# Optimization experiments

Hardware: AMD Instinct MI355X
Metric: run time of the kernel (lower is better)

## Reference

```python
import jax, jax.numpy as jnp
import numpy as np

N_NODES = 100000


def gcn_conv(x, edge_index, W, b):
    """PyG-style GCNConv: x' = D^-1/2 (A+I) D^-1/2 (x W) + b (self-loops added)."""
    n = x.shape[0]
    h = x @ W  # [N, out]
    loop = jnp.arange(n, dtype=edge_index.dtype)
    src = jnp.concatenate([edge_index[0], loop])  # [E+N]
    dst = jnp.concatenate([edge_index[1], loop])
    deg = jax.ops.segment_sum(jnp.ones_like(dst, dtype=h.dtype), dst, num_segments=n)
    dinv = jnp.where(deg > 0, jax.lax.rsqrt(deg), 0.0)
    norm = dinv[src] * dinv[dst]  # [E+N]
    # gather -> scale -> scatter-add aggregation
    out = jax.ops.segment_sum(norm[:, None] * h[src], dst, num_segments=n)
    return out + b


def setup_inputs() -> dict:
    key = jax.random.key(0)
    k1, k2, k3, k4 = jax.random.split(key, 4)
    n, e = N_NODES, 2560000
    x = jax.random.normal(k1, (n, 2), dtype=jnp.float32)
    edge_index = jax.random.randint(k2, (2, e), 0, n, dtype=jnp.int32)
    hidden = 32
    W1 = jax.random.normal(k3, (2, hidden), dtype=jnp.float32) * (1.0 / np.sqrt(2))
    b1 = jnp.zeros((hidden,), dtype=jnp.float32)
    W2 = jax.random.normal(k4, (hidden, 1), dtype=jnp.float32) * (1.0 / np.sqrt(hidden))
    b2 = jnp.zeros((1,), dtype=jnp.float32)
    return {"x": x, "edge_index": edge_index, "W1": W1, "b1": b1, "W2": W2, "b2": b2}


def reference(x, edge_index, W1, b1, W2, b2):
    h = jax.nn.relu(gcn_conv(x, edge_index, W1, b1))
    return gcn_conv(h, edge_index, W2, b2)  # [N, 1]
```

## Files before the change

kernel.cpp:

```cpp
#include <hip/hip_runtime.h>


#define NBMAX 1024
#define NRMAX 32
#define AGG_BLKS 16
#define CHUNK 4096
#define NCHP 640
#define DBITS 12
#define DMASK 4095
#define NOEDGE 0xFFFFFFFFu


__device__ __forceinline__ int block_scan_excl(int v, int tid, int* wtot ) {
    int lane = tid & 63, w = tid >> 6;
    int inc = v;
#pragma unroll
    for (int d = 1; d < 64; d <<= 1) {
        int u = __shfl_up(inc, d);
        if (lane >= d) inc += u;
    }
    if (lane == 63) wtot[w] = inc;
    __syncthreads();
    if (w == 0) {
        int t = (lane < 16) ? wtot[lane] : 0;
#pragma unroll
        for (int d = 1; d < 16; d <<= 1) {
            int u = __shfl_up(t, d);
            if (lane >= d) t += u;
        }
        if (lane < 16) wtot[lane] = t;
        if (lane == 15) wtot[16] = t;
    }
    __syncthreads();
    int base = (w > 0) ? wtot[w - 1] : 0;
    return base + inc - v;
}


__global__ void k_px(const float2* __restrict__ x, const int* __restrict__ pdeg,
                     float* __restrict__ dinv, float2* __restrict__ px, int n) {
    int i = blockIdx.x * blockDim.x + threadIdx.x;
    if (i >= n) return;
    int deg = 1;
#pragma unroll
    for (int b = 0; b < AGG_BLKS; ++b) deg += pdeg[b * n + i];
    float d = rsqrtf((float)deg);
    dinv[i] = d;
    float2 xv = x[i];
    px[i] = make_float2(d * xv.x, d * xv.y);
}

__global__ void k_node(const float2* __restrict__ px, const float2* __restrict__ pP,
                       const float* __restrict__ dinv,
                       const float* __restrict__ W1, const float* __restrict__ b1,
                       const float* __restrict__ W2, float* __restrict__ s, int n) {
    int i = blockIdx.x * blockDim.x + threadIdx.x;
    if (i >= n) return;
    float2 v = px[i];
    float ax = v.x, ay = v.y;
#pragma unroll
    for (int b = 0; b < AGG_BLKS; ++b) {
        float2 p = pP[b * n + i];
        ax += p.x; ay += p.y;
    }
    float d = dinv[i];
    float dot = 0.f;
#pragma unroll
    for (int j = 0; j < 32; ++j) {
        float acc = fmaf(ax, W1[j], ay * W1[32 + j]);
        float h = fmaxf(fmaf(d, acc, b1[j]), 0.f);
        dot = fmaf(h, W2[j], dot);
    }
    s[i] = d * dot;
}

__global__ void k_out(const float* __restrict__ s, const float* __restrict__ ps,
                      const float* __restrict__ dinv, const float* __restrict__ b2,
                      float* __restrict__ out, int n) {
    int i = blockIdx.x * blockDim.x + threadIdx.x;
    if (i >= n) return;
    float acc = s[i];
#pragma unroll
    for (int b = 0; b < AGG_BLKS; ++b) acc += ps[b * n + i];
    out[i] = dinv[i] * acc + b2[0];
}


__global__ void k_cnt(const int* __restrict__ src, const int* __restrict__ dst,
                      int* __restrict__ cntT, int e, int NS, int NB) {
    __shared__ int h[NBMAX];
    for (int t = threadIdx.x; t < NB; t += blockDim.x) h[t] = 0;
    __syncthreads();
    int c0 = blockIdx.x * CHUNK, c1 = min(c0 + CHUNK, e);
    int len = c1 - c0, lq = len >> 2;
    const int4* d4 = (const int4*)(dst + c0);
    const int4* s4 = (const int4*)(src + c0);
    for (int j = threadIdx.x; j < lq; j += blockDim.x) {
        int4 dv = d4[j], sv = s4[j];
        atomicAdd(&h[(dv.x >> DBITS) * NS + (sv.x >> DBITS)], 1);
        atomicAdd(&h[(dv.y >> DBITS) * NS + (sv.y >> DBITS)], 1);
        atomicAdd(&h[(dv.z >> DBITS) * NS + (sv.z >> DBITS)], 1);
        atomicAdd(&h[(dv.w >> DBITS) * NS + (sv.w >> DBITS)], 1);
    }
    if (threadIdx.x == 0)
        for (int i = lq * 4; i < len; ++i)
            atomicAdd(&h[(dst[c0 + i] >> DBITS) * NS + (src[c0 + i] >> DBITS)], 1);
    __syncthreads();
    for (int t = threadIdx.x; t < NB; t += blockDim.x)
        cntT[blockIdx.x * NBMAX + t] = h[t];
}

__global__ __launch_bounds__(1024)
void k_scanA(int* __restrict__ cntT, int* __restrict__ tot, int NCH) {
    __shared__ int wtot[17];
    int bin = blockIdx.x, tid = threadIdx.x;
    int v = (tid < NCH) ? cntT[tid * NBMAX + bin] : 0;
    int ex = block_scan_excl(v, tid, wtot);
    if (tid < NCH) cntT[tid * NBMAX + bin] = ex;
    if (tid == 0) tot[bin] = wtot[16];
}

__global__ __launch_bounds__(1024)
void k_scanB(const int* __restrict__ tot, int* __restrict__ gbin,
             int* __restrict__ rbase, int* __restrict__ rlenp,
             unsigned* __restrict__ packed, int NB, int NS) {
    __shared__ int wtot[17];
    int tid = threadIdx.x;
    int t = (tid < NB) ? tot[tid] : 0;
    int p = (t + 3) & ~3;
    int gb = block_scan_excl(p, tid, wtot);
    int totalp = wtot[16];
    if (tid < NB) {
        gbin[tid] = gb;
        for (int k = t; k < p; ++k) packed[gb + k] = NOEDGE;
    }
    __syncthreads();
    if (tid < NB && (tid % NS) == 0) {
        int r = tid / NS;
        rbase[r] = gb;
        int nxt = (tid + NS < NB) ? gbin[tid + NS] : totalp;
        rlenp[r] = nxt - gb;
    }
}

__global__ __launch_bounds__(1024)
void k_bscatter(const int* __restrict__ src, const int* __restrict__ dst,
                const int* __restrict__ ofsT, const int* __restrict__ tot,
                const int* __restrict__ gbin, unsigned* __restrict__ packed,
                int e, int NS, int NB, int NCH) {
    __shared__ int curx[NBMAX], gba[NBMAX];
    __shared__ unsigned sbuf[CHUNK];
    __shared__ int dest[CHUNK];
    __shared__ int wtot[17];
    int blk = blockIdx.x, tid = threadIdx.x;
    int c0 = blk * CHUNK, c1 = min(c0 + CHUNK, e);
    int len = c1 - c0, lq = len >> 2;
    int cur = 0, hv = 0;
    if (tid < NB) {
        cur = ofsT[blk * NBMAX + tid];
        int nxt = (blk + 1 < NCH) ? ofsT[(blk + 1) * NBMAX + tid] : tot[tid];
        hv = nxt - cur;
    }
    int lo = block_scan_excl(hv, tid, wtot);
    if (tid < NB) {
        curx[tid] = lo;
        gba[tid] = gbin[tid] + cur - lo;
    }
    __syncthreads();
    const int4* d4 = (const int4*)(dst + c0);
    const int4* s4 = (const int4*)(src + c0);
    for (int j = tid; j < lq; j += blockDim.x) {
        int4 dv = d4[j], sv = s4[j];
        {
            int b = (dv.x >> DBITS) * NS + (sv.x >> DBITS);
            int sl = atomicAdd(&curx[b], 1);
            sbuf[sl] = ((unsigned)sv.x << DBITS) | (unsigned)(dv.x & DMASK);
            dest[sl] = gba[b] + sl;
        }
        {
            int b = (dv.y >> DBITS) * NS + (sv.y >> DBITS);
            int sl = atomicAdd(&curx[b], 1);
            sbuf[sl] = ((unsigned)sv.y << DBITS) | (unsigned)(dv.y & DMASK);
            dest[sl] = gba[b] + sl;
        }
        {
            int b = (dv.z >> DBITS) * NS + (sv.z >> DBITS);
            int sl = atomicAdd(&curx[b], 1);
            sbuf[sl] = ((unsigned)sv.z << DBITS) | (unsigned)(dv.z & DMASK);
            dest[sl] = gba[b] + sl;
        }
        {
            int b = (dv.w >> DBITS) * NS + (sv.w >> DBITS);
            int sl = atomicAdd(&curx[b], 1);
            sbuf[sl] = ((unsigned)sv.w << DBITS) | (unsigned)(dv.w & DMASK);
            dest[sl] = gba[b] + sl;
        }
    }
    if (tid == 0)
        for (int i = lq * 4; i < len; ++i) {
            int d = dst[c0 + i], sx = src[c0 + i];
            int b = (d >> DBITS) * NS + (sx >> DBITS);
            int sl = atomicAdd(&curx[b], 1);
            sbuf[sl] = ((unsigned)sx << DBITS) | (unsigned)(d & DMASK);
            dest[sl] = gba[b] + sl;
        }
    __syncthreads();
    for (int t = tid; t < len; t += blockDim.x)
        packed[dest[t]] = sbuf[t];
}


__global__ __launch_bounds__(1024, 8)
void k_deg(const unsigned* __restrict__ packed, const int* __restrict__ rbase,
           const int* __restrict__ rlenp, int* __restrict__ pdeg, int n) {
    __shared__ int acc[DMASK + 1];
    int r = blockIdx.y, b = blockIdx.x;
    int rs_r = min(DMASK + 1, n - (r << DBITS));
    for (int t = threadIdx.x; t < rs_r; t += blockDim.x) acc[t] = 0;
    __syncthreads();
    int base = rbase[r], q = rlenp[r] >> 2;
    int qper = (q + gridDim.x - 1) / gridDim.x;
    int qlo = b * qper, qhi = min(qlo + qper, q);
    const uint4* p4 = (const uint4*)(packed + base);
    for (int j = qlo + threadIdx.x; j < qhi; j += blockDim.x) {
        uint4 v = p4[j];
        if (v.x != NOEDGE) atomicAdd(&acc[v.x & DMASK], 1);
        if (v.y != NOEDGE) atomicAdd(&acc[v.y & DMASK], 1);
        if (v.z != NOEDGE) atomicAdd(&acc[v.z & DMASK], 1);
        if (v.w != NOEDGE) atomicAdd(&acc[v.w & DMASK], 1);
    }
    __syncthreads();
    int nb = b * n + (r << DBITS);
    for (int t = threadIdx.x; t < rs_r; t += blockDim.x) pdeg[nb + t] = acc[t];
}

__global__ __launch_bounds__(1024, 8)
void k_agg1(const unsigned* __restrict__ packed, const int* __restrict__ rbase,
            const int* __restrict__ rlenp, const float2* __restrict__ px,
            float2* __restrict__ pP, int n) {
    __shared__ float acc[2 * (DMASK + 1)];
    int r = blockIdx.y, b = blockIdx.x;
    int rs_r = min(DMASK + 1, n - (r << DBITS));
    for (int t = threadIdx.x; t < 2 * rs_r; t += blockDim.x) acc[t] = 0.f;
    __syncthreads();
    int base = rbase[r], q = rlenp[r] >> 2;
    int qper = (q + gridDim.x - 1) / gridDim.x;
    int qlo = b * qper, qhi = min(qlo + qper, q);
    const uint4* p4 = (const uint4*)(packed + base);
    int nm1 = n - 1;
    for (int j = qlo + threadIdx.x; j < qhi; j += blockDim.x) {
        uint4 v = p4[j];
        int i0 = min((int)(v.x >> DBITS), nm1);
        int i1 = min((int)(v.y >> DBITS), nm1);
        int i2 = min((int)(v.z >> DBITS), nm1);
        int i3 = min((int)(v.w >> DBITS), nm1);
        float2 g0 = px[i0], g1 = px[i1], g2 = px[i2], g3 = px[i3];
        if (v.x != NOEDGE) { int d0 = (v.x & DMASK) * 2; atomicAdd(&acc[d0], g0.x); atomicAdd(&acc[d0 + 1], g0.y); }
        if (v.y != NOEDGE) { int d1 = (v.y & DMASK) * 2; atomicAdd(&acc[d1], g1.x); atomicAdd(&acc[d1 + 1], g1.y); }
        if (v.z != NOEDGE) { int d2 = (v.z & DMASK) * 2; atomicAdd(&acc[d2], g2.x); atomicAdd(&acc[d2 + 1], g2.y); }
        if (v.w != NOEDGE) { int d3 = (v.w & DMASK) * 2; atomicAdd(&acc[d3], g3.x); atomicAdd(&acc[d3 + 1], g3.y); }
    }
    __syncthreads();
    int nb = b * n + (r << DBITS);
    for (int t = threadIdx.x; t < rs_r; t += blockDim.x)
        pP[nb + t] = make_float2(acc[2 * t], acc[2 * t + 1]);
}

__global__ __launch_bounds__(1024, 8)
void k_agg2(const unsigned* __restrict__ packed, const int* __restrict__ rbase,
            const int* __restrict__ rlenp, const float* __restrict__ s,
            float* __restrict__ ps, int n) {
    __shared__ float acc[DMASK + 1];
    int r = blockIdx.y, b = blockIdx.x;
    int rs_r = min(DMASK + 1, n - (r << DBITS));
    for (int t = threadIdx.x; t < rs_r; t += blockDim.x) acc[t] = 0.f;
    __syncthreads();
    int base = rbase[r], q = rlenp[r] >> 2;
    int qper = (q + gridDim.x - 1) / gridDim.x;
    int qlo = b * qper, qhi = min(qlo + qper, q);
    const uint4* p4 = (const uint4*)(packed + base);
    int nm1 = n - 1;
    for (int j = qlo + threadIdx.x; j < qhi; j += blockDim.x) {
        uint4 v = p4[j];
        int i0 = min((int)(v.x >> DBITS), nm1);
        int i1 = min((int)(v.y >> DBITS), nm1);
        int i2 = min((int)(v.z >> DBITS), nm1);
        int i3 = min((int)(v.w >> DBITS), nm1);
        float g0 = s[i0], g1 = s[i1], g2 = s[i2], g3 = s[i3];
        if (v.x != NOEDGE) atomicAdd(&acc[v.x & DMASK], g0);
        if (v.y != NOEDGE) atomicAdd(&acc[v.y & DMASK], g1);
        if (v.z != NOEDGE) atomicAdd(&acc[v.z & DMASK], g2);
        if (v.w != NOEDGE) atomicAdd(&acc[v.w & DMASK], g3);
    }
    __syncthreads();
    int nb = b * n + (r << DBITS);
    for (int t = threadIdx.x; t < rs_r; t += blockDim.x) ps[nb + t] = acc[t];
}


__global__ void f_zero(int* __restrict__ ideg, float2* __restrict__ P, int n) {
    int i = blockIdx.x * blockDim.x + threadIdx.x;
    if (i < n) { ideg[i] = 0; P[i] = make_float2(0.f, 0.f); }
}
__global__ void f_count(const int* __restrict__ dst, int* __restrict__ ideg, int e) {
    int i = blockIdx.x * blockDim.x + threadIdx.x;
    if (i < e) atomicAdd(&ideg[dst[i]], 1);
}
__global__ void f_px(const float2* __restrict__ x, const int* __restrict__ ideg,
                     float* __restrict__ dinv, float2* __restrict__ px, int n) {
    int i = blockIdx.x * blockDim.x + threadIdx.x;
    if (i >= n) return;
    float d = rsqrtf((float)(1 + ideg[i]));
    dinv[i] = d;
    float2 xv = x[i];
    px[i] = make_float2(d * xv.x, d * xv.y);
}
__global__ void f_scatter_px(const int* __restrict__ src, const int* __restrict__ dst,
                             const float2* __restrict__ px, float* __restrict__ Pf, int e) {
    int i = blockIdx.x * blockDim.x + threadIdx.x;
    if (i >= e) return;
    int sidx = src[i], d = dst[i];
    float2 v = px[sidx];
    atomicAdd(&Pf[2 * d], v.x);
    atomicAdd(&Pf[2 * d + 1], v.y);
}
__global__ void f_node(const float2* __restrict__ px, const float2* __restrict__ P,
                       const float* __restrict__ dinv,
                       const float* __restrict__ W1, const float* __restrict__ b1,
                       const float* __restrict__ W2,
                       float* __restrict__ s, float* __restrict__ S, int n) {
    int i = blockIdx.x * blockDim.x + threadIdx.x;
    if (i >= n) return;
    float d = dinv[i];
    float2 v = px[i], p = P[i];
    float ax = v.x + p.x, ay = v.y + p.y;
    float dot = 0.f;
#pragma unroll
    for (int j = 0; j < 32; ++j) {
        float acc = fmaf(ax, W1[j], ay * W1[32 + j]);
        float h = fmaxf(fmaf(d, acc, b1[j]), 0.f);
        dot = fmaf(h, W2[j], dot);
    }
    float sv = d * dot;
    s[i] = sv;
    S[i] = sv;
}
__global__ void f_scatter_s(const int* __restrict__ src, const int* __restrict__ dst,
                            const float* __restrict__ s, float* __restrict__ S, int e) {
    int i = blockIdx.x * blockDim.x + threadIdx.x;
    if (i < e) atomicAdd(&S[dst[i]], s[src[i]]);
}
__global__ void f_out(const float* __restrict__ S, const float* __restrict__ dinv,
                      const float* __restrict__ b2, float* __restrict__ out, int n) {
    int i = blockIdx.x * blockDim.x + threadIdx.x;
    if (i < n) out[i] = dinv[i] * S[i] + b2[0];
}


extern "C" void kernel_launch(void* const* d_in, const int* in_sizes, int n_in,
                              void* d_out, int out_size, void* d_ws, size_t ws_size,
                              hipStream_t stream) {
    const float* x  = (const float*)d_in[0];
    const int*   ei = (const int*)d_in[1];
    const float* W1 = (const float*)d_in[2];
    const float* b1 = (const float*)d_in[3];
    const float* W2 = (const float*)d_in[4];
    const float* b2 = (const float*)d_in[5];
    float* out = (float*)d_out;

    int n = in_sizes[0] / 2;
    int e = in_sizes[1] / 2;
    const int* src = ei;
    const int* dst = ei + e;
    int NR  = (n + DMASK) >> DBITS;
    int NS  = NR;
    int NB  = NR * NS;
    int NCH = (e + CHUNK - 1) / CHUNK;

    char* ws = (char*)d_ws;
    auto align = [](size_t v) { return (v + 255) & ~(size_t)255; };
    size_t off = 0;
    float*  dinv = (float*) (ws + off); off = align(off + (size_t)n * 4);
    float2* px   = (float2*)(ws + off); off = align(off + (size_t)n * 8);
    float*  s    = (float*) (ws + off); off = align(off + (size_t)n * 4);
    int*    pdeg = (int*)   (ws + off); off = align(off + (size_t)AGG_BLKS * n * 4);
    float2* pP   = (float2*)(ws + off); off = align(off + (size_t)AGG_BLKS * n * 8);
    float*  ps   = (float*) (ws + off); off = align(off + (size_t)AGG_BLKS * n * 4);
    int*    rbase = (int*)(ws + off); off = align(off + NRMAX * 4);
    int*    rlenp = (int*)(ws + off); off = align(off + NRMAX * 4);
    int*    gbin  = (int*)(ws + off); off = align(off + NBMAX * 4);
    int*    tot   = (int*)(ws + off); off = align(off + NBMAX * 4);
    int*    cntT  = (int*)(ws + off); off = align(off + (size_t)NCHP * NBMAX * 4);
    unsigned* packed = (unsigned*)(ws + off);
    size_t need = off + (size_t)(e + 4 * NBMAX) * 4;

    const int B = 256;
    int gn = (n + B - 1) / B, ge = (e + B - 1) / B;

    bool fast = (need <= ws_size) && (NB <= NBMAX) && (NCH <= NCHP) && (NR <= NRMAX);

    if (fast) {
        dim3 ag(AGG_BLKS, NR);
        k_cnt     <<<NCH, B, 0, stream>>>(src, dst, cntT, e, NS, NB);
        k_scanA   <<<NB, 1024, 0, stream>>>(cntT, tot, NCH);
        k_scanB   <<<1, 1024, 0, stream>>>(tot, gbin, rbase, rlenp, packed, NB, NS);
        k_bscatter<<<NCH, 1024, 0, stream>>>(src, dst, cntT, tot, gbin, packed, e, NS, NB, NCH);
        k_deg     <<<ag, 1024, 0, stream>>>(packed, rbase, rlenp, pdeg, n);
        k_px      <<<gn, B, 0, stream>>>((const float2*)x, pdeg, dinv, px, n);
        k_agg1    <<<ag, 1024, 0, stream>>>(packed, rbase, rlenp, px, pP, n);
        k_node    <<<gn, B, 0, stream>>>(px, pP, dinv, W1, b1, W2, s, n);
        k_agg2    <<<ag, 1024, 0, stream>>>(packed, rbase, rlenp, s, ps, n);
        k_out     <<<gn, B, 0, stream>>>(s, ps, dinv, b2, out, n);
    } else {
        int*   ideg = pdeg;
        float2* P   = pP;
        float* S    = ps;
        f_zero      <<<gn, B, 0, stream>>>(ideg, P, n);
        f_count     <<<ge, B, 0, stream>>>(dst, ideg, e);
        f_px        <<<gn, B, 0, stream>>>((const float2*)x, ideg, dinv, px, n);
        f_scatter_px<<<ge, B, 0, stream>>>(src, dst, px, (float*)P, e);
        f_node      <<<gn, B, 0, stream>>>(px, P, dinv, W1, b1, W2, s, S, n);
        f_scatter_s <<<ge, B, 0, stream>>>(src, dst, s, S, e);
        f_out       <<<gn, B, 0, stream>>>(S, dinv, b2, out, n);
    }
}
```

Baseline: 110.2 us.

## Stage source-node windows in LDS for aggregation gathers via finer source binning

Source bins are narrowed to 2048 nodes (NS=49, NB=1225 bins), so each destination row's edges are grouped by source window. The aggregation kernels stage the matching px or s window into shared memory and read features from LDS instead of random global gathers. The price is more bins in the count, scan and scatter stages, a two-bins-per-thread scan, extra block syncs per window, and lower launch-bound occupancy hints for the aggregation kernels.

```diff
diff --git a/kernel.cpp b/kernel.cpp
--- a/kernel.cpp
+++ b/kernel.cpp
@@ -1,13 +1,15 @@
 #include <hip/hip_runtime.h>
 
 
-#define NBMAX 1024
+#define CSTR 1280
 #define NRMAX 32
 #define AGG_BLKS 16
 #define CHUNK 4096
 #define NCHP 640
 #define DBITS 12
 #define DMASK 4095
+#define SBITS 11
+#define SMASK 2047
 #define NOEDGE 0xFFFFFFFFu
 
 
@@ -88,7 +90,7 @@
 
 __global__ void k_cnt(const int* __restrict__ src, const int* __restrict__ dst,
                       int* __restrict__ cntT, int e, int NS, int NB) {
-    __shared__ int h[NBMAX];
+    __shared__ int h[CSTR];
     for (int t = threadIdx.x; t < NB; t += blockDim.x) h[t] = 0;
     __syncthreads();
     int c0 = blockIdx.x * CHUNK, c1 = min(c0 + CHUNK, e);
@@ -97,49 +99,57 @@
     const int4* s4 = (const int4*)(src + c0);
     for (int j = threadIdx.x; j < lq; j += blockDim.x) {
         int4 dv = d4[j], sv = s4[j];
-        atomicAdd(&h[(dv.x >> DBITS) * NS + (sv.x >> DBITS)], 1);
-        atomicAdd(&h[(dv.y >> DBITS) * NS + (sv.y >> DBITS)], 1);
-        atomicAdd(&h[(dv.z >> DBITS) * NS + (sv.z >> DBITS)], 1);
-        atomicAdd(&h[(dv.w >> DBITS) * NS + (sv.w >> DBITS)], 1);
+        atomicAdd(&h[(dv.x >> DBITS) * NS + (sv.x >> SBITS)], 1);
+        atomicAdd(&h[(dv.y >> DBITS) * NS + (sv.y >> SBITS)], 1);
+        atomicAdd(&h[(dv.z >> DBITS) * NS + (sv.z >> SBITS)], 1);
+        atomicAdd(&h[(dv.w >> DBITS) * NS + (sv.w >> SBITS)], 1);
     }
     if (threadIdx.x == 0)
         for (int i = lq * 4; i < len; ++i)
-            atomicAdd(&h[(dst[c0 + i] >> DBITS) * NS + (src[c0 + i] >> DBITS)], 1);
+            atomicAdd(&h[(dst[c0 + i] >> DBITS) * NS + (src[c0 + i] >> SBITS)], 1);
     __syncthreads();
     for (int t = threadIdx.x; t < NB; t += blockDim.x)
-        cntT[blockIdx.x * NBMAX + t] = h[t];
+        cntT[blockIdx.x * CSTR + t] = h[t];
 }
 
 __global__ __launch_bounds__(1024)
 void k_scanA(int* __restrict__ cntT, int* __restrict__ tot, int NCH) {
     __shared__ int wtot[17];
     int bin = blockIdx.x, tid = threadIdx.x;
-    int v = (tid < NCH) ? cntT[tid * NBMAX + bin] : 0;
+    int v = (tid < NCH) ? cntT[tid * CSTR + bin] : 0;
     int ex = block_scan_excl(v, tid, wtot);
-    if (tid < NCH) cntT[tid * NBMAX + bin] = ex;
+    if (tid < NCH) cntT[tid * CSTR + bin] = ex;
     if (tid == 0) tot[bin] = wtot[16];
 }
 
 __global__ __launch_bounds__(1024)
 void k_scanB(const int* __restrict__ tot, int* __restrict__ gbin,
              int* __restrict__ rbase, int* __restrict__ rlenp,
-             unsigned* __restrict__ packed, int NB, int NS) {
+             unsigned* __restrict__ packed, int NB, int NS, int NR) {
     __shared__ int wtot[17];
+    __shared__ int gball[2048];
     int tid = threadIdx.x;
-    int t = (tid < NB) ? tot[tid] : 0;
-    int p = (t + 3) & ~3;
-    int gb = block_scan_excl(p, tid, wtot);
-    int totalp = wtot[16];
-    if (tid < NB) {
-        gbin[tid] = gb;
-        for (int k = t; k < p; ++k) packed[gb + k] = NOEDGE;
-    }
-    __syncthreads();
-    if (tid < NB && (tid % NS) == 0) {
-        int r = tid / NS;
-        rbase[r] = gb;
-        int nxt = (tid + NS < NB) ? gbin[tid + NS] : totalp;
-        rlenp[r] = nxt - gb;
+    int b0 = 2 * tid, b1 = b0 + 1;
+    int t0 = (b0 < NB) ? tot[b0] : 0;
+    int t1 = (b1 < NB) ? tot[b1] : 0;
+    int p0 = (t0 + 3) & ~3, p1 = (t1 + 3) & ~3;
+    int ps = block_scan_excl(p0 + p1, tid, wtot);
+    int total = wtot[16];
+    if (b0 < NB) {
+        gbin[b0] = ps; gball[b0] = ps;
+        for (int k = t0; k < p0; ++k) packed[ps + k] = NOEDGE;
+    }
+    if (b1 < NB) {
+        int base1 = ps + p0;
+        gbin[b1] = base1; gball[b1] = base1;
+        for (int k = t1; k < p1; ++k) packed[base1 + k] = NOEDGE;
+    }
+    __syncthreads();
+    if (tid < NR) {
+        int base = gball[tid * NS];
+        int nxt = (tid + 1 < NR) ? gball[(tid + 1) * NS] : total;
+        rbase[tid] = base;
+        rlenp[tid] = nxt - base;
     }
 }
 
@@ -148,60 +158,64 @@
                 const int* __restrict__ ofsT, const int* __restrict__ tot,
                 const int* __restrict__ gbin, unsigned* __restrict__ packed,
                 int e, int NS, int NB, int NCH) {
-    __shared__ int curx[NBMAX], gba[NBMAX];
+    __shared__ int curx[CSTR], gba[CSTR];
     __shared__ unsigned sbuf[CHUNK];
     __shared__ int dest[CHUNK];
     __shared__ int wtot[17];
     int blk = blockIdx.x, tid = threadIdx.x;
     int c0 = blk * CHUNK, c1 = min(c0 + CHUNK, e);
     int len = c1 - c0, lq = len >> 2;
-    int cur = 0, hv = 0;
-    if (tid < NB) {
-        cur = ofsT[blk * NBMAX + tid];
-        int nxt = (blk + 1 < NCH) ? ofsT[(blk + 1) * NBMAX + tid] : tot[tid];
-        hv = nxt - cur;
-    }
-    int lo = block_scan_excl(hv, tid, wtot);
-    if (tid < NB) {
-        curx[tid] = lo;
-        gba[tid] = gbin[tid] + cur - lo;
-    }
+    int b0 = 2 * tid, b1 = b0 + 1;
+    int cur0 = 0, cur1 = 0, h0 = 0, h1 = 0;
+    if (b0 < NB) {
+        cur0 = ofsT[blk * CSTR + b0];
+        int nxt = (blk + 1 < NCH) ? ofsT[(blk + 1) * CSTR + b0] : tot[b0];
+        h0 = nxt - cur0;
+    }
+    if (b1 < NB) {
+        cur1 = ofsT[blk * CSTR + b1];
+        int nxt = (blk + 1 < NCH) ? ofsT[(blk + 1) * CSTR + b1] : tot[b1];
+        h1 = nxt - cur1;
+    }
+    int lo = block_scan_excl(h0 + h1, tid, wtot);
+    if (b0 < NB) { curx[b0] = lo;      gba[b0] = gbin[b0] + cur0 - lo; }
+    if (b1 < NB) { curx[b1] = lo + h0; gba[b1] = gbin[b1] + cur1 - (lo + h0); }
     __syncthreads();
     const int4* d4 = (const int4*)(dst + c0);
     const int4* s4 = (const int4*)(src + c0);
     for (int j = tid; j < lq; j += blockDim.x) {
         int4 dv = d4[j], sv = s4[j];
         {
-            int b = (dv.x >> DBITS) * NS + (sv.x >> DBITS);
+            int b = (dv.x >> DBITS) * NS + (sv.x >> SBITS);
             int sl = atomicAdd(&curx[b], 1);
-            sbuf[sl] = ((unsigned)sv.x << DBITS) | (unsigned)(dv.x & DMASK);
+            sbuf[sl] = ((unsigned)(sv.x & SMASK) << DBITS) | (unsigned)(dv.x & DMASK);
             dest[sl] = gba[b] + sl;
         }
         {
-            int b = (dv.y >> DBITS) * NS + (sv.y >> DBITS);
+            int b = (dv.y >> DBITS) * NS + (sv.y >> SBITS);
             int sl = atomicAdd(&curx[b], 1);
-            sbuf[sl] = ((unsigned)sv.y << DBITS) | (unsigned)(dv.y & DMASK);
+            sbuf[sl] = ((unsigned)(sv.y & SMASK) << DBITS) | (unsigned)(dv.y & DMASK);
             dest[sl] = gba[b] + sl;
         }
         {
-            int b = (dv.z >> DBITS) * NS + (sv.z >> DBITS);
+            int b = (dv.z >> DBITS) * NS + (sv.z >> SBITS);
             int sl = atomicAdd(&curx[b], 1);
-            sbuf[sl] = ((unsigned)sv.z << DBITS) | (unsigned)(dv.z & DMASK);
+            sbuf[sl] = ((unsigned)(sv.z & SMASK) << DBITS) | (unsigned)(dv.z & DMASK);
             dest[sl] = gba[b] + sl;
         }
         {
-            int b = (dv.w >> DBITS) * NS + (sv.w >> DBITS);
+            int b = (dv.w >> DBITS) * NS + (sv.w >> SBITS);
             int sl = atomicAdd(&curx[b], 1);
-            sbuf[sl] = ((unsigned)sv.w << DBITS) | (unsigned)(dv.w & DMASK);
+            sbuf[sl] = ((unsigned)(sv.w & SMASK) << DBITS) | (unsigned)(dv.w & DMASK);
             dest[sl] = gba[b] + sl;
         }
     }
     if (tid == 0)
         for (int i = lq * 4; i < len; ++i) {
             int d = dst[c0 + i], sx = src[c0 + i];
-            int b = (d >> DBITS) * NS + (sx >> DBITS);
+            int b = (d >> DBITS) * NS + (sx >> SBITS);
             int sl = atomicAdd(&curx[b], 1);
-            sbuf[sl] = ((unsigned)sx << DBITS) | (unsigned)(d & DMASK);
+            sbuf[sl] = ((unsigned)(sx & SMASK) << DBITS) | (unsigned)(d & DMASK);
             dest[sl] = gba[b] + sl;
         }
     __syncthreads();
@@ -234,67 +248,97 @@
     for (int t = threadIdx.x; t < rs_r; t += blockDim.x) pdeg[nb + t] = acc[t];
 }
 
-__global__ __launch_bounds__(1024, 8)
-void k_agg1(const unsigned* __restrict__ packed, const int* __restrict__ rbase,
-            const int* __restrict__ rlenp, const float2* __restrict__ px,
-            float2* __restrict__ pP, int n) {
+__global__ __launch_bounds__(1024, 2)
+void k_agg1(const unsigned* __restrict__ packed, const int* __restrict__ gbin,
+            const int* __restrict__ rbase, const int* __restrict__ rlenp,
+            const float2* __restrict__ px, float2* __restrict__ pP,
+            int n, int NS) {
     __shared__ float acc[2 * (DMASK + 1)];
-    int r = blockIdx.y, b = blockIdx.x;
+    __shared__ float2 win[SMASK + 1];
+    __shared__ int gb[64];
+    int r = blockIdx.y, b = blockIdx.x, tid = threadIdx.x;
     int rs_r = min(DMASK + 1, n - (r << DBITS));
-    for (int t = threadIdx.x; t < 2 * rs_r; t += blockDim.x) acc[t] = 0.f;
-    __syncthreads();
-    int base = rbase[r], q = rlenp[r] >> 2;
+    for (int t = tid; t < 2 * rs_r; t += blockDim.x) acc[t] = 0.f;
+    int rb = rbase[r], rl = rlenp[r];
+    if (tid <= NS) gb[tid] = (tid == NS) ? rb + rl : gbin[r * NS + tid];
+    __syncthreads();
+    int q = rl >> 2;
     int qper = (q + gridDim.x - 1) / gridDim.x;
-    int qlo = b * qper, qhi = min(qlo + qper, q);
-    const uint4* p4 = (const uint4*)(packed + base);
-    int nm1 = n - 1;
-    for (int j = qlo + threadIdx.x; j < qhi; j += blockDim.x) {
-        uint4 v = p4[j];
-        int i0 = min((int)(v.x >> DBITS), nm1);
-        int i1 = min((int)(v.y >> DBITS), nm1);
-        int i2 = min((int)(v.z >> DBITS), nm1);
-        int i3 = min((int)(v.w >> DBITS), nm1);
-        float2 g0 = px[i0], g1 = px[i1], g2 = px[i2], g3 = px[i3];
-        if (v.x != NOEDGE) { int d0 = (v.x & DMASK) * 2; atomicAdd(&acc[d0], g0.x); atomicAdd(&acc[d0 + 1], g0.y); }
-        if (v.y != NOEDGE) { int d1 = (v.y & DMASK) * 2; atomicAdd(&acc[d1], g1.x); atomicAdd(&acc[d1 + 1], g1.y); }
-        if (v.z != NOEDGE) { int d2 = (v.z & DMASK) * 2; atomicAdd(&acc[d2], g2.x); atomicAdd(&acc[d2 + 1], g2.y); }
-        if (v.w != NOEDGE) { int d3 = (v.w & DMASK) * 2; atomicAdd(&acc[d3], g3.x); atomicAdd(&acc[d3 + 1], g3.y); }
-    }
-    __syncthreads();
+    int qlo = min(b * qper, q), qhi = min(qlo + qper, q);
+    int e0 = rb + qlo * 4, e1 = rb + qhi * 4;
+    int k0 = 0;
+    while (k0 + 1 < NS && gb[k0 + 1] <= e0) ++k0;
+    for (int k = k0; k < NS && gb[k] < e1; ++k) {
+        int lo = max(gb[k], e0), hi = min(gb[k + 1], e1);
+        if (lo >= hi) continue;
+        int wb = k << SBITS;
+        int wlen = min(SMASK + 1, n - wb);
+        for (int t = tid; t < wlen; t += blockDim.x) win[t] = px[wb + t];
+        __syncthreads();
+        const uint4* p4 = (const uint4*)(packed + lo);
+        int nq = (hi - lo) >> 2;
+        for (int j = tid; j < nq; j += blockDim.x) {
+            uint4 v = p4[j];
+            float2 g0 = win[(v.x >> DBITS) & SMASK];
+            float2 g1 = win[(v.y >> DBITS) & SMASK];
+            float2 g2 = win[(v.z >> DBITS) & SMASK];
+            float2 g3 = win[(v.w >> DBITS) & SMASK];
+            if (v.x != NOEDGE) { int d0 = (v.x & DMASK) * 2; atomicAdd(&acc[d0], g0.x); atomicAdd(&acc[d0 + 1], g0.y); }
+            if (v.y != NOEDGE) { int d1 = (v.y & DMASK) * 2; atomicAdd(&acc[d1], g1.x); atomicAdd(&acc[d1 + 1], g1.y); }
+            if (v.z != NOEDGE) { int d2 = (v.z & DMASK) * 2; atomicAdd(&acc[d2], g2.x); atomicAdd(&acc[d2 + 1], g2.y); }
+            if (v.w != NOEDGE) { int d3 = (v.w & DMASK) * 2; atomicAdd(&acc[d3], g3.x); atomicAdd(&acc[d3 + 1], g3.y); }
+        }
+        __syncthreads();
+    }
     int nb = b * n + (r << DBITS);
-    for (int t = threadIdx.x; t < rs_r; t += blockDim.x)
+    for (int t = tid; t < rs_r; t += blockDim.x)
         pP[nb + t] = make_float2(acc[2 * t], acc[2 * t + 1]);
 }
 
-__global__ __launch_bounds__(1024, 8)
-void k_agg2(const unsigned* __restrict__ packed, const int* __restrict__ rbase,
-            const int* __restrict__ rlenp, const float* __restrict__ s,
-            float* __restrict__ ps, int n) {
+__global__ __launch_bounds__(1024, 4)
+void k_agg2(const unsigned* __restrict__ packed, const int* __restrict__ gbin,
+            const int* __restrict__ rbase, const int* __restrict__ rlenp,
+            const float* __restrict__ s, float* __restrict__ ps,
+            int n, int NS) {
     __shared__ float acc[DMASK + 1];
-    int r = blockIdx.y, b = blockIdx.x;
+    __shared__ float win[SMASK + 1];
+    __shared__ int gb[64];
+    int r = blockIdx.y, b = blockIdx.x, tid = threadIdx.x;
     int rs_r = min(DMASK + 1, n - (r << DBITS));
-    for (int t = threadIdx.x; t < rs_r; t += blockDim.x) acc[t] = 0.f;
-    __syncthreads();
-    int base = rbase[r], q = rlenp[r] >> 2;
+    for (int t = tid; t < rs_r; t += blockDim.x) acc[t] = 0.f;
+    int rb = rbase[r], rl = rlenp[r];
+    if (tid <= NS) gb[tid] = (tid == NS) ? rb + rl : gbin[r * NS + tid];
+    __syncthreads();
+    int q = rl >> 2;
     int qper = (q + gridDim.x - 1) / gridDim.x;
-    int qlo = b * qper, qhi = min(qlo + qper, q);
-    const uint4* p4 = (const uint4*)(packed + base);
-    int nm1 = n - 1;
-    for (int j = qlo + threadIdx.x; j < qhi; j += blockDim.x) {
-        uint4 v = p4[j];
-        int i0 = min((int)(v.x >> DBITS), nm1);
-        int i1 = min((int)(v.y >> DBITS), nm1);
-        int i2 = min((int)(v.z >> DBITS), nm1);
-        int i3 = min((int)(v.w >> DBITS), nm1);
-        float g0 = s[i0], g1 = s[i1], g2 = s[i2], g3 = s[i3];
-        if (v.x != NOEDGE) atomicAdd(&acc[v.x & DMASK], g0);
-        if (v.y != NOEDGE) atomicAdd(&acc[v.y & DMASK], g1);
-        if (v.z != NOEDGE) atomicAdd(&acc[v.z & DMASK], g2);
-        if (v.w != NOEDGE) atomicAdd(&acc[v.w & DMASK], g3);
-    }
-    __syncthreads();
+    int qlo = min(b * qper, q), qhi = min(qlo + qper, q);
+    int e0 = rb + qlo * 4, e1 = rb + qhi * 4;
+    int k0 = 0;
+    while (k0 + 1 < NS && gb[k0 + 1] <= e0) ++k0;
+    for (int k = k0; k < NS && gb[k] < e1; ++k) {
+        int lo = max(gb[k], e0), hi = min(gb[k + 1], e1);
+        if (lo >= hi) continue;
+        int wb = k << SBITS;
+        int wlen = min(SMASK + 1, n - wb);
+        for (int t = tid; t < wlen; t += blockDim.x) win[t] = s[wb + t];
+        __syncthreads();
+        const uint4* p4 = (const uint4*)(packed + lo);
+        int nq = (hi - lo) >> 2;
+        for (int j = tid; j < nq; j += blockDim.x) {
+            uint4 v = p4[j];
+            float g0 = win[(v.x >> DBITS) & SMASK];
+            float g1 = win[(v.y >> DBITS) & SMASK];
+            float g2 = win[(v.z >> DBITS) & SMASK];
+            float g3 = win[(v.w >> DBITS) & SMASK];
+            if (v.x != NOEDGE) atomicAdd(&acc[v.x & DMASK], g0);
+            if (v.y != NOEDGE) atomicAdd(&acc[v.y & DMASK], g1);
+            if (v.z != NOEDGE) atomicAdd(&acc[v.z & DMASK], g2);
+            if (v.w != NOEDGE) atomicAdd(&acc[v.w & DMASK], g3);
+        }
+        __syncthreads();
+    }
     int nb = b * n + (r << DBITS);
-    for (int t = threadIdx.x; t < rs_r; t += blockDim.x) ps[nb + t] = acc[t];
+    for (int t = tid; t < rs_r; t += blockDim.x) ps[nb + t] = acc[t];
 }
 
 
@@ -373,7 +417,7 @@
     const int* src = ei;
     const int* dst = ei + e;
     int NR  = (n + DMASK) >> DBITS;
-    int NS  = NR;
+    int NS  = (n + SMASK) >> SBITS;
     int NB  = NR * NS;
     int NCH = (e + CHUNK - 1) / CHUNK;
 
@@ -388,28 +432,29 @@
     float*  ps   = (float*) (ws + off); off = align(off + (size_t)AGG_BLKS * n * 4);
     int*    rbase = (int*)(ws + off); off = align(off + NRMAX * 4);
     int*    rlenp = (int*)(ws + off); off = align(off + NRMAX * 4);
-    int*    gbin  = (int*)(ws + off); off = align(off + NBMAX * 4);
-    int*    tot   = (int*)(ws + off); off = align(off + NBMAX * 4);
-    int*    cntT  = (int*)(ws + off); off = align(off + (size_t)NCHP * NBMAX * 4);
+    int*    gbin  = (int*)(ws + off); off = align(off + 2048 * 4);
+    int*    tot   = (int*)(ws + off); off = align(off + 2048 * 4);
+    int*    cntT  = (int*)(ws + off); off = align(off + (size_t)NCHP * CSTR * 4);
     unsigned* packed = (unsigned*)(ws + off);
-    size_t need = off + (size_t)(e + 4 * NBMAX) * 4;
+    size_t need = off + (size_t)(e + 4 * CSTR) * 4;
 
     const int B = 256;
     int gn = (n + B - 1) / B, ge = (e + B - 1) / B;
 
-    bool fast = (need <= ws_size) && (NB <= NBMAX) && (NCH <= NCHP) && (NR <= NRMAX);
+    bool fast = (need <= ws_size) && (NB <= CSTR) && (NCH <= NCHP) &&
+                (NR <= NRMAX) && (NS <= 63);
 
     if (fast) {
         dim3 ag(AGG_BLKS, NR);
         k_cnt     <<<NCH, B, 0, stream>>>(src, dst, cntT, e, NS, NB);
         k_scanA   <<<NB, 1024, 0, stream>>>(cntT, tot, NCH);
-        k_scanB   <<<1, 1024, 0, stream>>>(tot, gbin, rbase, rlenp, packed, NB, NS);
+        k_scanB   <<<1, 1024, 0, stream>>>(tot, gbin, rbase, rlenp, packed, NB, NS, NR);
         k_bscatter<<<NCH, 1024, 0, stream>>>(src, dst, cntT, tot, gbin, packed, e, NS, NB, NCH);
         k_deg     <<<ag, 1024, 0, stream>>>(packed, rbase, rlenp, pdeg, n);
         k_px      <<<gn, B, 0, stream>>>((const float2*)x, pdeg, dinv, px, n);
-        k_agg1    <<<ag, 1024, 0, stream>>>(packed, rbase, rlenp, px, pP, n);
+        k_agg1    <<<ag, 1024, 0, stream>>>(packed, gbin, rbase, rlenp, px, pP, n, NS);
         k_node    <<<gn, B, 0, stream>>>(px, pP, dinv, W1, b1, W2, s, n);
-        k_agg2    <<<ag, 1024, 0, stream>>>(packed, rbase, rlenp, s, ps, n);
+        k_agg2    <<<ag, 1024, 0, stream>>>(packed, gbin, rbase, rlenp, s, ps, n, NS);
         k_out     <<<gn, B, 0, stream>>>(s, ps, dinv, b2, out, n);
     } else {
         int*   ideg = pdeg;
```

Result: slower. 138.0 us (+25.2%).
